# Performance work log

Measured on AMD Instinct MI355X. Metric: run time of the kernel, lower is better.

Reference implementation:

```python
import jax, jax.numpy as jnp
import numpy as np

DT = 0.01
MIN_VARIANCE = 0.01
REG_WEIGHT = 0.01
EPS = 1e-06


def setup_inputs() -> dict:
    key = jax.random.key(0)
    k1, k2, k3, k4 = jax.random.split(key, 4)
    B, T = 256, 16384
    return {
        "vel_pred": jax.random.normal(k1, (B, T, 2), dtype=jnp.float32),
        "cov_pred": jax.random.normal(k2, (B, T, 2), dtype=jnp.float32),
        "vel_gt": jax.random.normal(k3, (B, T, 2), dtype=jnp.float32),
        "pos_gt": jax.random.normal(k4, (B, T, 2), dtype=jnp.float32),
        "log_delta_v": jnp.zeros((), dtype=jnp.float32),
        "log_delta_c": jnp.zeros((), dtype=jnp.float32),
    }


def reference(vel_pred, cov_pred, vel_gt, pos_gt, log_delta_v, log_delta_c):
    # Sequential loop pos[t] = pos[t-1] + vel_pred[t-1]*dt, pos[0] = vel_pred[0]*dt
    # == dt * (vel_pred[:, 0:1] + exclusive_cumsum_T(vel_pred))  -- a parallel scan.
    excl = jnp.concatenate(
        [jnp.zeros_like(vel_pred[:, :1]), jnp.cumsum(vel_pred[:, :-1], axis=1)], axis=1
    )
    pos_pred = (vel_pred[:, :1] + excl) * DT  # [B, T, 2]

    lv_p = jnp.mean((pos_pred - pos_gt) ** 2)
    lv_e = jnp.mean((vel_pred - vel_gt) ** 2)
    lv_total = lv_p + lv_e

    sigma = jnp.clip(jnp.exp(cov_pred), MIN_VARIANCE, None)  # [B, T, 2] diag cov
    inv_sigma = 1.0 / sigma
    diff = vel_gt - vel_pred
    mahal = jnp.sum(inv_sigma * diff ** 2, axis=-1)  # [B, T]
    log_det = jnp.log(sigma[..., 0] * sigma[..., 1] + EPS)
    lc_total = 0.5 * jnp.mean(mahal + log_det)

    delta_v = jnp.exp(log_delta_v)
    delta_c = jnp.exp(log_delta_c)
    total_loss = (
        lv_total / (2.0 * delta_v ** 2)
        + lc_total / (2.0 * delta_c ** 2)
        + log_delta_v
        + log_delta_c
    )
    reg = jnp.mean(jnp.sum(inv_sigma, axis=-1))
    total_loss = total_loss + REG_WEIGHT * reg
    return total_loss
```

## Files before the change

kernel.cpp:

```cpp
#include <hip/hip_runtime.h>

static constexpr int B_ = 256;
static constexpr int T_ = 16384;
static constexpr int TPB = 1024;
static constexpr int F4_ROW = T_ * 2 / 4;
static constexpr int CHUNKS = F4_ROW / TPB;

static constexpr float DTc    = 0.01f;
static constexpr float MINVAR = 0.01f;
static constexpr float EPSc   = 1e-6f;


__device__ __forceinline__ float waveReduce(float v) {
#pragma unroll
  for (int d = 32; d > 0; d >>= 1) v += __shfl_down(v, d, 64);
  return v;
}
__device__ __forceinline__ double waveReduceD(double v) {
#pragma unroll
  for (int d = 32; d > 0; d >>= 1) v += __shfl_down(v, d, 64);
  return v;
}

__global__ __launch_bounds__(TPB) void fusedKern(
    const float4* __restrict__ vel, const float4* __restrict__ cov,
    const float4* __restrict__ vgt, const float4* __restrict__ pgt,
    float* __restrict__ pPos, float* __restrict__ pLve,
    float* __restrict__ pLc,  float* __restrict__ pReg) {
  const int b = blockIdx.x;
  const int tid = threadIdx.x;
  const int lane = tid & 63, wid = tid >> 6;
  const int rowbase = b * F4_ROW;

  __shared__ float2 wt[2][16];
  __shared__ float  sh[4][16];

  const float2 v0 = ((const float2*)vel)[b * T_];

  float runx = 0.f, runy = 0.f;
  float lve = 0.f, lc = 0.f, reg = 0.f, apos = 0.f;

  float4 v = vel[rowbase + tid];
  float4 c = cov[rowbase + tid];
  float4 g = vgt[rowbase + tid];
  float4 p = pgt[rowbase + tid];

  for (int ch = 0; ch < CHUNKS; ++ch) {
    float4 nv, nc, ng, np;
    const bool more = (ch + 1 < CHUNKS);
    if (more) {
      int idx = rowbase + (ch + 1) * TPB + tid;
      nv = vel[idx]; nc = cov[idx]; ng = vgt[idx]; np = pgt[idx];
    }

    {
      float dx = g.x - v.x, dy = g.y - v.y;
      float sqx = dx * dx, sqy = dy * dy;
      lve += sqx + sqy;
      float sx = fmaxf(__expf(c.x), MINVAR);
      float sy = fmaxf(__expf(c.y), MINVAR);
      float ixv = 1.0f / sx, iyv = 1.0f / sy;
      lc += ixv * sqx + iyv * sqy + __logf(sx * sy + EPSc);
      reg += ixv + iyv;
    }
    {
      float dx = g.z - v.z, dy = g.w - v.w;
      float sqx = dx * dx, sqy = dy * dy;
      lve += sqx + sqy;
      float sx = fmaxf(__expf(c.z), MINVAR);
      float sy = fmaxf(__expf(c.w), MINVAR);
      float ixv = 1.0f / sx, iyv = 1.0f / sy;
      lc += ixv * sqx + iyv * sqy + __logf(sx * sy + EPSc);
      reg += ixv + iyv;
    }

    const float sx = v.x + v.z, sy = v.y + v.w;
    float ix = sx, iy = sy;
#pragma unroll
    for (int d = 1; d < 64; d <<= 1) {
      float ux = __shfl_up(ix, (unsigned)d, 64);
      float uy = __shfl_up(iy, (unsigned)d, 64);
      if (lane >= d) { ix += ux; iy += uy; }
    }
    const int slot = ch & 1;
    if (lane == 63) wt[slot][wid] = make_float2(ix, iy);
    __syncthreads();

    float offx = ix - sx + runx, offy = iy - sy + runy;
    float ctx = 0.f, cty = 0.f;
#pragma unroll
    for (int w = 0; w < 16; ++w) {
      float2 t = wt[slot][w];
      if (w < wid) { offx += t.x; offy += t.y; }
      ctx += t.x; cty += t.y;
    }

    {
      float px = DTc * (v0.x + offx), py = DTc * (v0.y + offy);
      float ex = px - p.x, ey = py - p.y;
      apos += ex * ex + ey * ey;
      float bx2 = offx + v.x, by2 = offy + v.y;
      px = DTc * (v0.x + bx2); py = DTc * (v0.y + by2);
      ex = px - p.z; ey = py - p.w;
      apos += ex * ex + ey * ey;
    }

    runx += ctx; runy += cty;
    if (more) { v = nv; c = nc; g = ng; p = np; }
  }

  float r0 = waveReduce(apos);
  float r1 = waveReduce(lve);
  float r2 = waveReduce(lc);
  float r3 = waveReduce(reg);
  __syncthreads();
  if (lane == 0) { sh[0][wid] = r0; sh[1][wid] = r1; sh[2][wid] = r2; sh[3][wid] = r3; }
  __syncthreads();
  if (tid == 0) {
    float t0 = 0.f, t1 = 0.f, t2 = 0.f, t3 = 0.f;
#pragma unroll
    for (int w = 0; w < 16; ++w) { t0 += sh[0][w]; t1 += sh[1][w]; t2 += sh[2][w]; t3 += sh[3][w]; }
    pPos[b] = t0; pLve[b] = t1; pLc[b] = t2; pReg[b] = t3;
  }
}

__global__ __launch_bounds__(256) void kernC(
    const float* __restrict__ pPos, const float* __restrict__ pLve,
    const float* __restrict__ pLc,  const float* __restrict__ pReg,
    const float* __restrict__ pldv, const float* __restrict__ pldc,
    float* __restrict__ out) {
  const int tid = threadIdx.x;
  const int lane = tid & 63, wid = tid >> 6;
  double a0 = (double)pPos[tid];
  double a1 = (double)pLve[tid];
  double a2 = (double)pLc[tid];
  double a3 = (double)pReg[tid];
  a0 = waveReduceD(a0);
  a1 = waveReduceD(a1);
  a2 = waveReduceD(a2);
  a3 = waveReduceD(a3);
  __shared__ double sh[4][4];
  if (lane == 0) { sh[0][wid] = a0; sh[1][wid] = a1; sh[2][wid] = a2; sh[3][wid] = a3; }
  __syncthreads();
  if (tid == 0) {
    double pos_sq = sh[0][0] + sh[0][1] + sh[0][2] + sh[0][3];
    double vel_sq = sh[1][0] + sh[1][1] + sh[1][2] + sh[1][3];
    double lcs    = sh[2][0] + sh[2][1] + sh[2][2] + sh[2][3];
    double regs   = sh[3][0] + sh[3][1] + sh[3][2] + sh[3][3];
    const double NBT2 = (double)B_ * (double)T_ * 2.0;
    const double NBT  = (double)B_ * (double)T_;
    double lv  = (pos_sq + vel_sq) / NBT2;
    double lc  = 0.5 * lcs / NBT;
    double reg = regs / NBT;
    double ldv = (double)pldv[0], ldc = (double)pldc[0];
    double total = lv / (2.0 * exp(2.0 * ldv)) + lc / (2.0 * exp(2.0 * ldc))
                 + ldv + ldc + 0.01 * reg;
    out[0] = (float)total;
  }
}

extern "C" void kernel_launch(void* const* d_in, const int* in_sizes, int n_in,
                              void* d_out, int out_size, void* d_ws, size_t ws_size,
                              hipStream_t stream) {
  const float4* vel = (const float4*)d_in[0];
  const float4* cov = (const float4*)d_in[1];
  const float4* vgt = (const float4*)d_in[2];
  const float4* pgt = (const float4*)d_in[3];
  const float* ldv = (const float*)d_in[4];
  const float* ldc = (const float*)d_in[5];

  char* ws = (char*)d_ws;
  float* pPos = (float*)ws;
  float* pLve = (float*)(ws + 1024);
  float* pLc  = (float*)(ws + 2048);
  float* pReg = (float*)(ws + 3072);

  fusedKern<<<B_, TPB, 0, stream>>>(vel, cov, vgt, pgt, pPos, pLve, pLc, pReg);
  kernC<<<1, 256, 0, stream>>>(pPos, pLve, pLc, pReg, ldv, ldc, (float*)d_out);
}
```

Before: 159.8 us.

## Replace chunked block scan with per-thread serial scan and single block scan

Instead of looping over 8 chunks, each doing a wave scan plus a block-level barrier, every thread now owns 8 contiguous float4s, computes a serial local prefix in registers, and then performs one wave scan and one cross-wave scan. This removes 8 __syncthreads and repeated shuffle scans per row. In exchange, loads become strided per thread (each thread reads contiguous float4s, so adjacent lanes are 128B apart), which can hurt coalescing, and register pressure increases from holding 8 float4s plus prefix arrays.

```diff
diff --git a/kernel.cpp b/kernel.cpp
--- a/kernel.cpp
+++ b/kernel.cpp
@@ -4,7 +4,7 @@
 static constexpr int T_ = 16384;
 static constexpr int TPB = 1024;
 static constexpr int F4_ROW = T_ * 2 / 4;
-static constexpr int CHUNKS = F4_ROW / TPB;
+static constexpr int F4_THR = F4_ROW / TPB;
 
 static constexpr float DTc    = 0.01f;
 static constexpr float MINVAR = 0.01f;
@@ -30,31 +30,30 @@
   const int b = blockIdx.x;
   const int tid = threadIdx.x;
   const int lane = tid & 63, wid = tid >> 6;
-  const int rowbase = b * F4_ROW;
+  const int tbase = b * F4_ROW + tid * F4_THR;
 
-  __shared__ float2 wt[2][16];
-  __shared__ float  sh[4][16];
+  float4 v[F4_THR];
+#pragma unroll
+  for (int j = 0; j < F4_THR; ++j) v[j] = vel[tbase + j];
 
-  const float2 v0 = ((const float2*)vel)[b * T_];
+  float ex[F4_THR], ey[F4_THR];
+  float vx[F4_THR], vy[F4_THR];
+  float tx = 0.f, ty = 0.f;
+#pragma unroll
+  for (int j = 0; j < F4_THR; ++j) {
+    ex[j] = tx; ey[j] = ty;
+    vx[j] = v[j].x; vy[j] = v[j].y;
+    tx += v[j].x + v[j].z;
+    ty += v[j].y + v[j].w;
+  }
 
-  float runx = 0.f, runy = 0.f;
-  float lve = 0.f, lc = 0.f, reg = 0.f, apos = 0.f;
-
-  float4 v = vel[rowbase + tid];
-  float4 c = cov[rowbase + tid];
-  float4 g = vgt[rowbase + tid];
-  float4 p = pgt[rowbase + tid];
-
-  for (int ch = 0; ch < CHUNKS; ++ch) {
-    float4 nv, nc, ng, np;
-    const bool more = (ch + 1 < CHUNKS);
-    if (more) {
-      int idx = rowbase + (ch + 1) * TPB + tid;
-      nv = vel[idx]; nc = cov[idx]; ng = vgt[idx]; np = pgt[idx];
-    }
-
+  float lve = 0.f, lc = 0.f, reg = 0.f;
+#pragma unroll
+  for (int j = 0; j < F4_THR; ++j) {
+    float4 c = cov[tbase + j];
+    float4 g = vgt[tbase + j];
     {
-      float dx = g.x - v.x, dy = g.y - v.y;
+      float dx = g.x - v[j].x, dy = g.y - v[j].y;
       float sqx = dx * dx, sqy = dy * dy;
       lve += sqx + sqy;
       float sx = fmaxf(__expf(c.x), MINVAR);
@@ -64,7 +63,7 @@
       reg += ixv + iyv;
     }
     {
-      float dx = g.z - v.z, dy = g.w - v.w;
+      float dx = g.z - v[j].z, dy = g.w - v[j].w;
       float sqx = dx * dx, sqy = dy * dy;
       lve += sqx + sqy;
       float sx = fmaxf(__expf(c.z), MINVAR);
@@ -73,47 +72,54 @@
       lc += ixv * sqx + iyv * sqy + __logf(sx * sy + EPSc);
       reg += ixv + iyv;
     }
+  }
 
-    const float sx = v.x + v.z, sy = v.y + v.w;
-    float ix = sx, iy = sy;
+  float sx = tx, sy = ty;
 #pragma unroll
-    for (int d = 1; d < 64; d <<= 1) {
-      float ux = __shfl_up(ix, (unsigned)d, 64);
-      float uy = __shfl_up(iy, (unsigned)d, 64);
-      if (lane >= d) { ix += ux; iy += uy; }
-    }
-    const int slot = ch & 1;
-    if (lane == 63) wt[slot][wid] = make_float2(ix, iy);
-    __syncthreads();
+  for (int d = 1; d < 64; d <<= 1) {
+    float ux = __shfl_up(sx, (unsigned)d, 64);
+    float uy = __shfl_up(sy, (unsigned)d, 64);
+    if (lane >= d) { sx += ux; sy += uy; }
+  }
+  const float wxx = sx - tx, wxy = sy - ty;
 
-    float offx = ix - sx + runx, offy = iy - sy + runy;
-    float ctx = 0.f, cty = 0.f;
+  __shared__ float2 wt[16];
+  __shared__ float  sh[4][16];
+  if (lane == 63) wt[wid] = make_float2(sx, sy);
+  __syncthreads();
+
+  float ax = (lane < 16) ? wt[lane].x : 0.f;
+  float ay = (lane < 16) ? wt[lane].y : 0.f;
+  float iax = ax, iay = ay;
 #pragma unroll
-    for (int w = 0; w < 16; ++w) {
-      float2 t = wt[slot][w];
-      if (w < wid) { offx += t.x; offy += t.y; }
-      ctx += t.x; cty += t.y;
-    }
+  for (int d = 1; d < 16; d <<= 1) {
+    float ux = __shfl_up(iax, (unsigned)d, 64);
+    float uy = __shfl_up(iay, (unsigned)d, 64);
+    if (lane >= d) { iax += ux; iay += uy; }
+  }
+  const float bx0 = __shfl(iax - ax, wid, 64);
+  const float by0 = __shfl(iay - ay, wid, 64);
 
-    {
-      float px = DTc * (v0.x + offx), py = DTc * (v0.y + offy);
-      float ex = px - p.x, ey = py - p.y;
-      apos += ex * ex + ey * ey;
-      float bx2 = offx + v.x, by2 = offy + v.y;
-      px = DTc * (v0.x + bx2); py = DTc * (v0.y + by2);
-      ex = px - p.z; ey = py - p.w;
-      apos += ex * ex + ey * ey;
-    }
+  const float2 v0 = ((const float2*)vel)[b * T_];
 
-    runx += ctx; runy += cty;
-    if (more) { v = nv; c = nc; g = ng; p = np; }
+  float apos = 0.f;
+#pragma unroll
+  for (int j = 0; j < F4_THR; ++j) {
+    float4 q = pgt[tbase + j];
+    float px0 = bx0 + wxx + ex[j];
+    float py0 = by0 + wxy + ey[j];
+    float px = DTc * (v0.x + px0), py = DTc * (v0.y + py0);
+    float e0 = px - q.x, e1 = py - q.y;
+    apos += e0 * e0 + e1 * e1;
+    px = DTc * (v0.x + px0 + vx[j]); py = DTc * (v0.y + py0 + vy[j]);
+    e0 = px - q.z; e1 = py - q.w;
+    apos += e0 * e0 + e1 * e1;
   }
 
   float r0 = waveReduce(apos);
   float r1 = waveReduce(lve);
   float r2 = waveReduce(lc);
   float r3 = waveReduce(reg);
-  __syncthreads();
   if (lane == 0) { sh[0][wid] = r0; sh[1][wid] = r1; sh[2][wid] = r2; sh[3][wid] = r3; }
   __syncthreads();
   if (tid == 0) {
```

Measured after the change: 166.0 us. 1.04x slower.
